# Kernel optimization log

Hardware: AMD Instinct MI355X
Metric: run time of the kernel (lower is better)

## Reference

```python
import jax, jax.numpy as jnp
import numpy as np

N_PATCHES = 14
N_BLOCKS = 12
HIDDEN = 768
N_HEADS = 12
D_HEAD = HIDDEN // N_HEADS
MLP_RATIO = 4
OUT_D = 1000
BATCH = 32
C, H, W = 3, 224, 224
PS = H // N_PATCHES            # 16
INPUT_D = C * PS * PS          # 768
SEQ = N_PATCHES ** 2 + 1       # 197
LN_EPS = 1e-5


def _pos_emb(length, d):
    i = np.arange(length, dtype=np.float64)[:, None]
    j = np.arange(d, dtype=np.float64)[None, :]
    angle = i / (10000.0 ** ((j - (j % 2)) / d))
    pe = np.where(j % 2 == 0, np.sin(angle), np.cos(angle))
    return jnp.asarray(pe, dtype=jnp.float32)  # [length, d]


def setup_inputs() -> dict:
    key = jax.random.key(0)
    ks = jax.random.split(key, 16)
    s = 0.02
    inp = {
        "x": jax.random.normal(ks[0], (BATCH, C, H, W), jnp.float32),
        "W_map": jax.random.normal(ks[1], (INPUT_D, HIDDEN), jnp.float32) * s,
        "b_map": jnp.zeros((HIDDEN,), jnp.float32),
        "cls_tok": jax.random.uniform(ks[2], (1, HIDDEN), jnp.float32),
        "pos_emb": _pos_emb(SEQ, HIDDEN),
        "ln1_s": jnp.ones((N_BLOCKS, HIDDEN), jnp.float32),
        "ln1_b": jnp.zeros((N_BLOCKS, HIDDEN), jnp.float32),
        "Wq": jax.random.normal(ks[3], (N_BLOCKS, N_HEADS, D_HEAD, D_HEAD), jnp.float32) * s,
        "bq": jnp.zeros((N_BLOCKS, N_HEADS, D_HEAD), jnp.float32),
        "Wk": jax.random.normal(ks[4], (N_BLOCKS, N_HEADS, D_HEAD, D_HEAD), jnp.float32) * s,
        "bk": jnp.zeros((N_BLOCKS, N_HEADS, D_HEAD), jnp.float32),
        "Wv": jax.random.normal(ks[5], (N_BLOCKS, N_HEADS, D_HEAD, D_HEAD), jnp.float32) * s,
        "bv": jnp.zeros((N_BLOCKS, N_HEADS, D_HEAD), jnp.float32),
        "ln2_s": jnp.ones((N_BLOCKS, HIDDEN), jnp.float32),
        "ln2_b": jnp.zeros((N_BLOCKS, HIDDEN), jnp.float32),
        "W1": jax.random.normal(ks[6], (N_BLOCKS, HIDDEN, MLP_RATIO * HIDDEN), jnp.float32) * s,
        "b1": jnp.zeros((N_BLOCKS, MLP_RATIO * HIDDEN), jnp.float32),
        "W2": jax.random.normal(ks[7], (N_BLOCKS, MLP_RATIO * HIDDEN, HIDDEN), jnp.float32) * s,
        "b2": jnp.zeros((N_BLOCKS, HIDDEN), jnp.float32),
        "W_out": jax.random.normal(ks[8], (HIDDEN, OUT_D), jnp.float32) * s,
        "b_out": jnp.zeros((OUT_D,), jnp.float32),
    }
    return inp


def _layernorm(x, scale, bias):
    m = jnp.mean(x, axis=-1, keepdims=True)
    v = jnp.mean(jnp.square(x - m), axis=-1, keepdims=True)
    return (x - m) * jax.lax.rsqrt(v + LN_EPS) * scale + bias


def _patchify(x):
    # [N,C,H,W] -> [N, np*np, C*ps*ps], channel-major flatten per patch (matches torch flatten)
    n = x.shape[0]
    p = x.reshape(n, C, N_PATCHES, PS, N_PATCHES, PS)
    p = p.transpose(0, 2, 4, 1, 3, 5)  # [N, np, np, C, ps, ps]
    return p.reshape(n, N_PATCHES * N_PATCHES, INPUT_D)


def _msa(x, Wq, bq, Wk, bk, Wv, bv):
    # x: [N,S,D]; per-head separate linears, faithful scale = 1/sqrt(n_heads)
    n, s_, _ = x.shape
    xh = x.reshape(n, s_, N_HEADS, D_HEAD)
    q = jnp.einsum('nshd,hde->nhse', xh, Wq) + bq[None, :, None, :]
    k = jnp.einsum('nshd,hde->nhse', xh, Wk) + bk[None, :, None, :]
    v = jnp.einsum('nshd,hde->nhse', xh, Wv) + bv[None, :, None, :]
    scale = 1.0 / jnp.sqrt(jnp.float32(N_HEADS))
    att = jax.nn.softmax(jnp.einsum('nhse,nhte->nhst', q, k) * scale, axis=-1)
    o = jnp.einsum('nhst,nhte->nhse', att, v)
    return o.transpose(0, 2, 1, 3).reshape(n, s_, HIDDEN)


def reference(x, W_map, b_map, cls_tok, pos_emb, ln1_s, ln1_b, Wq, bq, Wk, bk, Wv, bv,
              ln2_s, ln2_b, W1, b1, W2, b2, W_out, b_out):
    n = x.shape[0]
    tokens = _patchify(x) @ W_map + b_map                       # [N, np^2, D]
    tokens = jnp.concatenate([jnp.broadcast_to(cls_tok[None], (n, 1, HIDDEN)), tokens], axis=1)
    h = tokens + pos_emb[None]                                  # [N, S, D]
    for blk in range(N_BLOCKS):
        attn_out = _msa(_layernorm(h, ln1_s[blk], ln1_b[blk]),
                        Wq[blk], bq[blk], Wk[blk], bk[blk], Wv[blk], bv[blk])
        out = h + attn_out
        # faithful to source: MLP branch reads norm2(x), not norm2(out)
        m = _layernorm(h, ln2_s[blk], ln2_b[blk])
        m = jax.nn.gelu(m @ W1[blk] + b1[blk], approximate=False) @ W2[blk] + b2[blk]
        h = out + m
    cls = h[:, 0]                                               # [N, D]
    return jax.nn.softmax(cls @ W_out + b_out, axis=1)          # [N, out_d]
```

## Files before the change

kernel.cpp:

```cpp
#include <hip/hip_runtime.h>
#include <math.h>

#define BATCH   32
#define SEQ     197
#define HIDDEN  768
#define NHEADS  12
#define DHEAD   64
#define NBLOCKS 12
#define MLP_D   3072
#define OUTD    1000
#define NPATCH  196
#define M_TOK   (BATCH*SEQ)
#define M_PAD   6400
#define LN_EPS  1e-5f
#define SP      208

typedef _Float16 f16;
typedef _Float16 f16x8 __attribute__((ext_vector_type(8)));
typedef _Float16 f16x4 __attribute__((ext_vector_type(4)));
typedef float    f32x4 __attribute__((ext_vector_type(4)));

__device__ __forceinline__ float gelu_exact(float x) {
    return 0.5f * x * (1.0f + erff(x * 0.70710678118654752f));
}

__device__ __forceinline__ void gload_lds16(const void* g, void* l) {
    __builtin_amdgcn_global_load_lds(
        (const __attribute__((address_space(1))) void*)g,
        (__attribute__((address_space(3))) void*)l, 16, 0, 0);
}

__device__ __forceinline__ f16x8 lds_ld(const char* base, int row, int rs, int kbyte) {
    return *(const f16x8*)(base + row*rs + (kbyte ^ ((row & 7) << 4)));
}

__global__ __launch_bounds__(256) void patchify_kernel(const float* __restrict__ x,
                                                       f16* __restrict__ patches) {
    int row = blockIdx.x;
    int n = row / NPATCH;
    int p = row % NPATCH;
    int pi = p / 14, pj = p % 14;
    for (int k = threadIdx.x; k < 768; k += 256) {
        int c   = k >> 8;
        int r   = (k >> 4) & 15;
        int col = k & 15;
        patches[(size_t)row*768 + k] =
            (f16)x[(((size_t)n*3 + c)*224 + (pi*16 + r))*224 + pj*16 + col];
    }
}

__global__ __launch_bounds__(256) void convtrans_kernel(const float* __restrict__ in,
                                                        f16* __restrict__ out,
                                                        int R, int C) {
    __shared__ float tile[32][33];
    int r0 = blockIdx.y * 32, c0 = blockIdx.x * 32;
    int tx = threadIdx.x & 31, ty = threadIdx.x >> 5;
    #pragma unroll
    for (int i = 0; i < 4; ++i) {
        int r = ty + i*8;
        tile[r][tx] = in[(size_t)(r0 + r)*C + c0 + tx];
    }
    __syncthreads();
    #pragma unroll
    for (int i = 0; i < 4; ++i) {
        int r = ty + i*8;
        out[(size_t)(c0 + r)*R + r0 + tx] = (f16)tile[tx][r];
    }
}

__global__ __launch_bounds__(256) void convtrans2_kernel(const float* __restrict__ W1,
                                                         const float* __restrict__ W2,
                                                         f16* __restrict__ W1T,
                                                         f16* __restrict__ W2T) {
    int z = blockIdx.z;
    const float* in = z ? W2 : W1;
    f16* out = z ? W2T : W1T;
    int R = z ? MLP_D : HIDDEN;
    int C = z ? HIDDEN : MLP_D;
    int bx = z ? blockIdx.y : blockIdx.x;
    int by = z ? blockIdx.x : blockIdx.y;
    __shared__ float tile[32][33];
    int r0 = by * 32, c0 = bx * 32;
    int tx = threadIdx.x & 31, ty = threadIdx.x >> 5;
    #pragma unroll
    for (int i = 0; i < 4; ++i) {
        int r = ty + i*8;
        tile[r][tx] = in[(size_t)(r0 + r)*C + c0 + tx];
    }
    __syncthreads();
    #pragma unroll
    for (int i = 0; i < 4; ++i) {
        int r = ty + i*8;
        out[(size_t)(c0 + r)*R + r0 + tx] = (f16)tile[tx][r];
    }
}

__global__ __launch_bounds__(256) void qkvtrans_kernel(const float* __restrict__ Wq,
                                                       const float* __restrict__ Wk,
                                                       const float* __restrict__ Wv,
                                                       f16* __restrict__ outT) {
    int b = blockIdx.x;
    int blkL = b / 36, rem = b % 36;
    int hh = rem / 3, mat = rem % 3;
    const float* in = (mat == 0 ? Wq : mat == 1 ? Wk : Wv) + ((size_t)(blkL*12 + hh))*4096;
    f16* out = outT + (size_t)b * 4096;
    __shared__ float tile[64][65];
    int t = threadIdx.x;
    for (int i = t; i < 4096; i += 256) tile[i >> 6][i & 63] = in[i];
    __syncthreads();
    for (int i = t; i < 4096; i += 256) out[i] = (f16)tile[i & 63][i >> 6];
}

__global__ __launch_bounds__(256) void assemble_kernel(const float* __restrict__ tokens,
                                                       const float* __restrict__ cls,
                                                       const float* __restrict__ pos,
                                                       float* __restrict__ h) {
    int r = blockIdx.x;
    int n = r / SEQ, s = r % SEQ;
    for (int c = threadIdx.x; c < 768; c += 256) {
        float v = (s == 0) ? cls[c] : tokens[(size_t)(n*NPATCH + s - 1)*768 + c];
        h[(size_t)r*768 + c] = v + pos[s*768 + c];
    }
}

__global__ __launch_bounds__(256) void layernorm2_kernel(const float* __restrict__ x,
                                                         const float* __restrict__ s1,
                                                         const float* __restrict__ b1,
                                                         const float* __restrict__ s2,
                                                         const float* __restrict__ b2,
                                                         f16* __restrict__ o1,
                                                         f16* __restrict__ o2) {
    int r = blockIdx.x;
    int t = threadIdx.x;
    const float* xr = x + (size_t)r*768;
    float v0 = xr[t], v1 = xr[t+256], v2 = xr[t+512];
    float s = v0 + v1 + v2;
    #pragma unroll
    for (int off = 32; off > 0; off >>= 1) s += __shfl_xor(s, off);
    __shared__ float red[4];
    int wid = t >> 6, lane = t & 63;
    if (lane == 0) red[wid] = s;
    __syncthreads();
    float mean = (red[0]+red[1]+red[2]+red[3]) * (1.0f/768.0f);
    __syncthreads();
    float d0 = v0-mean, d1 = v1-mean, d2 = v2-mean;
    float q = d0*d0 + d1*d1 + d2*d2;
    #pragma unroll
    for (int off = 32; off > 0; off >>= 1) q += __shfl_xor(q, off);
    if (lane == 0) red[wid] = q;
    __syncthreads();
    float var = (red[0]+red[1]+red[2]+red[3]) * (1.0f/768.0f);
    float inv = rsqrtf(var + LN_EPS);
    d0 *= inv; d1 *= inv; d2 *= inv;
    f16* p1 = o1 + (size_t)r*768;
    f16* p2 = o2 + (size_t)r*768;
    p1[t]     = (f16)(d0*s1[t]     + b1[t]);
    p1[t+256] = (f16)(d1*s1[t+256] + b1[t+256]);
    p1[t+512] = (f16)(d2*s1[t+512] + b1[t+512]);
    p2[t]     = (f16)(d0*s2[t]     + b2[t]);
    p2[t+256] = (f16)(d1*s2[t+256] + b2[t+256]);
    p2[t+512] = (f16)(d2*s2[t+512] + b2[t+512]);
}

__global__ __launch_bounds__(256) void fused_attn_kernel(
        const f16* __restrict__ lnh, const f16* __restrict__ qkvT,
        const float* __restrict__ bq, const float* __restrict__ bk,
        const float* __restrict__ bv, float* __restrict__ O) {
    int n = blockIdx.x, h = blockIdx.y;
    int t = threadIdx.x, wid = t >> 6, lane = t & 63;
    int lr = lane & 15;
    int lg = lane >> 4;

    __shared__ char lds[145408];
    char* Xs  = lds;
    char* Qs  = lds + 26624;
    char* Ks  = lds + 53248;
    char* VsT = lds + 79872;
    char* Ws  = lds + 112640;
    char* Ps  = lds + 112640 + wid*8192;

    const char* xsrc = (const char*)(lnh + (size_t)n*SEQ*768 + h*64);
    for (int c = t; c < SP*8; c += 256) {
        int s = c >> 3, kb = (c & 7) * 16;
        f16x8 v = {};
        if (s < SEQ) v = *(const f16x8*)(xsrc + (size_t)s*1536 + kb);
        *(f16x8*)(Xs + s*128 + (kb ^ ((s & 7) << 4))) = v;
    }
    const char* wsrc = (const char*)(qkvT) + (size_t)h * 3 * 4096 * 2;
    for (int c = t; c < 1536; c += 256) {
        int byte = c * 16, row = byte >> 7, kb = byte & 127;
        f16x8 v = *(const f16x8*)(wsrc + byte);
        *(f16x8*)(Ws + row*128 + (kb ^ ((row & 7) << 4))) = v;
    }
    for (int c = t; c < 384; c += 256) {
        int e = c / 6, sl = c % 6;
        int kb = 416 + sl * 16;
        *(f16x8*)(VsT + e*512 + (kb ^ ((e & 7) << 4))) = (f16x8){};
    }
    __syncthreads();

    for (int idx = wid; idx < 39; idx += 4) {
        int mat = idx / 13, mt = idx % 13;
        const float* bias = (mat == 0) ? bq : (mat == 1) ? bk : bv;
        #pragma unroll
        for (int nt = 0; nt < 4; ++nt) {
            f32x4 acc = {};
            #pragma unroll
            for (int ks = 0; ks < 2; ++ks) {
                f16x8 a = lds_ld(Xs, mt*16 + lr, 128, lg*16 + ks*64);
                f16x8 b = lds_ld(Ws, mat*64 + nt*16 + lr, 128, lg*16 + ks*64);
                acc = __builtin_amdgcn_mfma_f32_16x16x32_f16(a, b, acc, 0, 0, 0);
            }
            float bb = bias[h*64 + nt*16 + lr];
            if (mat < 2) {
                char* dst = (mat == 0) ? Qs : Ks;
                #pragma unroll
                for (int j = 0; j < 4; ++j) {
                    int s = mt*16 + lg*4 + j;
                    int eb = (nt*16 + lr) * 2;
                    *(f16*)(dst + s*128 + (eb ^ ((s & 7) << 4))) = (f16)(acc[j] + bb);
                }
            } else {
                int e = nt*16 + lr;
                int sb = (mt*16 + lg*4) * 2;
                f16x4 pv;
                #pragma unroll
                for (int j = 0; j < 4; ++j) pv[j] = (f16)(acc[j] + bb);
                *(f16x4*)(VsT + e*512 + (sb ^ ((e & 7) << 4))) = pv;
            }
        }
    }
    __syncthreads();

    for (int c = lane; c < 96; c += 64) {
        int r = c / 6, kb = 416 + (c % 6) * 16;
        *(f16x8*)(Ps + r*512 + (kb ^ ((r & 7) << 4))) = (f16x8){};
    }

    const float scale = 0.28867513459481288f;
    for (int mt = wid; mt < 13; mt += 4) {
        f32x4 sacc[13];
        #pragma unroll
        for (int nt = 0; nt < 13; ++nt) sacc[nt] = (f32x4){};
        #pragma unroll
        for (int ks = 0; ks < 2; ++ks) {
            f16x8 a = lds_ld(Qs, mt*16 + lr, 128, lg*16 + ks*64);
            #pragma unroll
            for (int nt = 0; nt < 13; ++nt) {
                f16x8 b = lds_ld(Ks, nt*16 + lr, 128, lg*16 + ks*64);
                sacc[nt] = __builtin_amdgcn_mfma_f32_16x16x32_f16(a, b, sacc[nt], 0, 0, 0);
            }
        }
        float mx0 = -1e30f, mx1 = -1e30f, mx2 = -1e30f, mx3 = -1e30f;
        #pragma unroll
        for (int nt = 0; nt < 13; ++nt) {
            bool valid = (nt*16 + lr) < SEQ;
            #pragma unroll
            for (int j = 0; j < 4; ++j) {
                float v = valid ? sacc[nt][j] * scale : -1e30f;
                sacc[nt][j] = v;
            }
            mx0 = fmaxf(mx0, sacc[nt][0]); mx1 = fmaxf(mx1, sacc[nt][1]);
            mx2 = fmaxf(mx2, sacc[nt][2]); mx3 = fmaxf(mx3, sacc[nt][3]);
        }
        #pragma unroll
        for (int off = 1; off < 16; off <<= 1) {
            mx0 = fmaxf(mx0, __shfl_xor(mx0, off));
            mx1 = fmaxf(mx1, __shfl_xor(mx1, off));
            mx2 = fmaxf(mx2, __shfl_xor(mx2, off));
            mx3 = fmaxf(mx3, __shfl_xor(mx3, off));
        }
        float s0 = 0.f, s1 = 0.f, s2 = 0.f, s3 = 0.f;
        #pragma unroll
        for (int nt = 0; nt < 13; ++nt) {
            float p0 = expf(sacc[nt][0] - mx0); sacc[nt][0] = p0; s0 += p0;
            float p1 = expf(sacc[nt][1] - mx1); sacc[nt][1] = p1; s1 += p1;
            float p2 = expf(sacc[nt][2] - mx2); sacc[nt][2] = p2; s2 += p2;
            float p3 = expf(sacc[nt][3] - mx3); sacc[nt][3] = p3; s3 += p3;
        }
        #pragma unroll
        for (int off = 1; off < 16; off <<= 1) {
            s0 += __shfl_xor(s0, off); s1 += __shfl_xor(s1, off);
            s2 += __shfl_xor(s2, off); s3 += __shfl_xor(s3, off);
        }
        float i0 = 1.0f/s0, i1 = 1.0f/s1, i2 = 1.0f/s2, i3 = 1.0f/s3;
        #pragma unroll
        for (int nt = 0; nt < 13; ++nt) {
            int cb = (nt*16 + lr) * 2;
            { int r = lg*4 + 0; *(f16*)(Ps + r*512 + (cb ^ ((r & 7) << 4))) = (f16)(sacc[nt][0] * i0); }
            { int r = lg*4 + 1; *(f16*)(Ps + r*512 + (cb ^ ((r & 7) << 4))) = (f16)(sacc[nt][1] * i1); }
            { int r = lg*4 + 2; *(f16*)(Ps + r*512 + (cb ^ ((r & 7) << 4))) = (f16)(sacc[nt][2] * i2); }
            { int r = lg*4 + 3; *(f16*)(Ps + r*512 + (cb ^ ((r & 7) << 4))) = (f16)(sacc[nt][3] * i3); }
        }
        f32x4 oacc[4] = {};
        #pragma unroll
        for (int ks = 0; ks < 8; ++ks) {
            f16x8 a = lds_ld(Ps, lr, 512, lg*16 + ks*64);
            #pragma unroll
            for (int nt = 0; nt < 4; ++nt) {
                f16x8 b = lds_ld(VsT, nt*16 + lr, 512, lg*16 + ks*64);
                oacc[nt] = __builtin_amdgcn_mfma_f32_16x16x32_f16(a, b, oacc[nt], 0, 0, 0);
            }
        }
        #pragma unroll
        for (int nt = 0; nt < 4; ++nt) {
            #pragma unroll
            for (int j = 0; j < 4; ++j) {
                int s = mt*16 + lg*4 + j;
                if (s < SEQ)
                    O[((size_t)(n*SEQ + s))*768 + h*64 + nt*16 + lr] = oacc[nt][j];
            }
        }
    }
}

template<int MODE>
__global__ __launch_bounds__(256) void hgemm_kernel(
        const f16* __restrict__ A,
        const f16* __restrict__ BT,
        const float* __restrict__ bias,
        const float* __restrict__ res1,
        const float* __restrict__ res2,
        void* __restrict__ Cout, int M, int N, int K, int nbx) {
    __shared__ f16 As[2][128*64];
    __shared__ f16 Bs[2][64*64];
    int t = threadIdx.x;
    int wid = t >> 6, lane = t & 63;
    int lr = lane & 15, lg = lane >> 4;
    int wr = wid >> 1, wc = wid & 1;

    int nwg = gridDim.x, bid = blockIdx.x;
    int q = nwg >> 3, r = nwg & 7;
    int xcd = bid & 7, idx = bid >> 3;
    int swz = (xcd < r) ? xcd*(q+1) + idx : r*(q+1) + (xcd-r)*q + idx;
    int bn = (swz % nbx) * 64;
    int bm = (swz / nbx) * 128;

    int arow[4], aswk[4];
    #pragma unroll
    for (int i = 0; i < 4; ++i) {
        int fb = i*4096 + wid*1024 + lane*16;
        int row = fb >> 7, slot = (fb >> 4) & 7;
        arow[i] = row; aswk[i] = (slot ^ (row & 7)) * 8;
    }

    #define STAGE(P, K0)                                                          \
        do {                                                                      \
            _Pragma("unroll")                                                     \
            for (int i = 0; i < 4; ++i)                                           \
                gload_lds16(A + (size_t)(bm + arow[i])*K + (K0) + aswk[i],        \
                            (char*)&As[P][0] + i*4096 + wid*1024);                \
            _Pragma("unroll")                                                     \
            for (int i = 0; i < 2; ++i)                                           \
                gload_lds16(BT + (size_t)(bn + arow[i])*K + (K0) + aswk[i],       \
                            (char*)&Bs[P][0] + i*4096 + wid*1024);                \
        } while (0)

    f32x4 acc[4][2] = {};
    int nk = K >> 6;

    STAGE(0, 0);
    __syncthreads();
    for (int kt = 0; kt < nk; ++kt) {
        int cur = kt & 1;
        if (kt + 1 < nk) STAGE(cur ^ 1, (kt + 1) * 64);
        const char* Ab = (const char*)&As[cur][0];
        const char* Bb = (const char*)&Bs[cur][0];
        #pragma unroll
        for (int ks = 0; ks < 2; ++ks) {
            f16x8 a[4], b[2];
            #pragma unroll
            for (int m = 0; m < 4; ++m)
                a[m] = lds_ld(Ab, wr*64 + m*16 + lr, 128, lg*16 + ks*64);
            #pragma unroll
            for (int nn = 0; nn < 2; ++nn)
                b[nn] = lds_ld(Bb, wc*32 + nn*16 + lr, 128, lg*16 + ks*64);
            #pragma unroll
            for (int m = 0; m < 4; ++m)
                #pragma unroll
                for (int nn = 0; nn < 2; ++nn)
                    acc[m][nn] = __builtin_amdgcn_mfma_f32_16x16x32_f16(a[m], b[nn], acc[m][nn], 0, 0, 0);
        }
        __syncthreads();
    }
    #undef STAGE

    int row0 = bm + wr*64 + lg*4;
    int col0 = bn + wc*32 + lr;
    #pragma unroll
    for (int m = 0; m < 4; ++m) {
        #pragma unroll
        for (int nn = 0; nn < 2; ++nn) {
            int col = col0 + nn*16;
            float bv = bias[col];
            #pragma unroll
            for (int j = 0; j < 4; ++j) {
                int row = row0 + m*16 + j;
                if (row >= M) continue;
                float v = acc[m][nn][j] + bv;
                size_t idx = (size_t)row*N + col;
                if (MODE == 0) {
                    if (res1) v += res1[idx] + res2[idx];
                    ((float*)Cout)[idx] = v;
                } else {
                    ((f16*)Cout)[idx] = (f16)gelu_exact(v);
                }
            }
        }
    }
}

__global__ __launch_bounds__(256) void head_kernel(const float* __restrict__ h,
                                                   const float* __restrict__ W_out,
                                                   const float* __restrict__ b_out,
                                                   float* __restrict__ out) {
    int n = blockIdx.x, t = threadIdx.x;
    __shared__ float xs[HIDDEN];
    __shared__ float red[4];
    const float* hr = h + (size_t)n*SEQ*HIDDEN;
    for (int k = t; k < HIDDEN; k += 256) xs[k] = hr[k];
    __syncthreads();

    bool v3 = t < (OUTD - 768);
    int c3 = v3 ? (t + 768) : t;
    float a0 = 0.f, a1 = 0.f, a2 = 0.f, a3 = 0.f;
    #pragma unroll 8
    for (int k = 0; k < HIDDEN; ++k) {
        float xv = xs[k];
        const float* wr = W_out + (size_t)k*OUTD;
        a0 = fmaf(xv, wr[t],       a0);
        a1 = fmaf(xv, wr[t + 256], a1);
        a2 = fmaf(xv, wr[t + 512], a2);
        a3 = fmaf(xv, wr[c3],      a3);
    }
    a0 += b_out[t]; a1 += b_out[t + 256]; a2 += b_out[t + 512];
    a3 = v3 ? (a3 + b_out[t + 768]) : -1e30f;

    int wid = t >> 6, lane = t & 63;
    float mx = fmaxf(fmaxf(a0, a1), fmaxf(a2, a3));
    #pragma unroll
    for (int off = 32; off > 0; off >>= 1) mx = fmaxf(mx, __shfl_xor(mx, off));
    if (lane == 0) red[wid] = mx;
    __syncthreads();
    mx = fmaxf(fmaxf(red[0], red[1]), fmaxf(red[2], red[3]));
    __syncthreads();

    float p0 = expf(a0 - mx), p1 = expf(a1 - mx), p2 = expf(a2 - mx);
    float p3 = v3 ? expf(a3 - mx) : 0.f;
    float s = p0 + p1 + p2 + p3;
    #pragma unroll
    for (int off = 32; off > 0; off >>= 1) s += __shfl_xor(s, off);
    if (lane == 0) red[wid] = s;
    __syncthreads();
    s = red[0] + red[1] + red[2] + red[3];
    float inv = 1.0f / s;

    float* orow = out + (size_t)n*OUTD;
    orow[t]       = p0 * inv;
    orow[t + 256] = p1 * inv;
    orow[t + 512] = p2 * inv;
    if (v3) orow[t + 768] = p3 * inv;
}

extern "C" void kernel_launch(void* const* d_in, const int* in_sizes, int n_in,
                              void* d_out, int out_size, void* d_ws, size_t ws_size,
                              hipStream_t stream) {
    const float* x     = (const float*)d_in[0];
    const float* W_map = (const float*)d_in[1];
    const float* b_map = (const float*)d_in[2];
    const float* cls_t = (const float*)d_in[3];
    const float* pos   = (const float*)d_in[4];
    const float* ln1_s = (const float*)d_in[5];
    const float* ln1_b = (const float*)d_in[6];
    const float* Wq    = (const float*)d_in[7];
    const float* bq    = (const float*)d_in[8];
    const float* Wk    = (const float*)d_in[9];
    const float* bk    = (const float*)d_in[10];
    const float* Wv    = (const float*)d_in[11];
    const float* bv    = (const float*)d_in[12];
    const float* ln2_s = (const float*)d_in[13];
    const float* ln2_b = (const float*)d_in[14];
    const float* W1    = (const float*)d_in[15];
    const float* b1    = (const float*)d_in[16];
    const float* W2    = (const float*)d_in[17];
    const float* b2    = (const float*)d_in[18];
    const float* W_out = (const float*)d_in[19];
    const float* b_out = (const float*)d_in[20];
    float* out = (float*)d_out;

    char* w = (char*)d_ws;
    const size_t SZ32 = (size_t)M_TOK * HIDDEN * 4;
    float* h        = (float*)w;  w += SZ32;
    float* attn_out = (float*)w;  w += SZ32;
    f16*   mid_h    = (f16*)w;    w += (size_t)M_PAD * MLP_D * 2;
    f16*   lnh1     = (f16*)w;    w += (size_t)M_PAD * HIDDEN * 2;
    f16*   lnh2     = (f16*)w;    w += (size_t)M_PAD * HIDDEN * 2;
    f16*   W1T      = (f16*)w;    w += (size_t)MLP_D * HIDDEN * 2;
    f16*   W2T      = (f16*)w;    w += (size_t)HIDDEN * MLP_D * 2;
    f16*   WmapT    = (f16*)w;    w += (size_t)768 * 768 * 2;
    f16*   qkvT     = (f16*)w;    w += (size_t)NBLOCKS * NHEADS * 3 * 64 * 64 * 2;

    f16* patches_h = mid_h;
    patchify_kernel<<<BATCH*NPATCH, 256, 0, stream>>>(x, patches_h);
    {
        dim3 g(768/32, 768/32);
        convtrans_kernel<<<g, 256, 0, stream>>>(W_map, WmapT, 768, 768);
    }
    qkvtrans_kernel<<<NBLOCKS*NHEADS*3, 256, 0, stream>>>(Wq, Wk, Wv, qkvT);
    hgemm_kernel<0><<<49*12, 256, 0, stream>>>(patches_h, WmapT, b_map,
                                               nullptr, nullptr,
                                               (void*)attn_out, BATCH*NPATCH, 768, 768, 12);
    assemble_kernel<<<M_TOK, 256, 0, stream>>>(attn_out, cls_t, pos, h);

    for (int blk = 0; blk < NBLOCKS; ++blk) {
        layernorm2_kernel<<<M_TOK, 256, 0, stream>>>(h,
            ln1_s + blk*768, ln1_b + blk*768, ln2_s + blk*768, ln2_b + blk*768,
            lnh1, lnh2);
        {
            dim3 g(MLP_D/32, HIDDEN/32, 2);
            convtrans2_kernel<<<g, 256, 0, stream>>>(W1 + (size_t)blk*HIDDEN*MLP_D,
                                                     W2 + (size_t)blk*MLP_D*HIDDEN, W1T, W2T);
        }
        {
            dim3 g(BATCH, NHEADS);
            fused_attn_kernel<<<g, 256, 0, stream>>>(lnh1,
                qkvT + (size_t)blk*NHEADS*3*4096,
                bq + (size_t)blk*768, bk + (size_t)blk*768, bv + (size_t)blk*768,
                attn_out);
        }
        hgemm_kernel<1><<<50*48, 256, 0, stream>>>(lnh2, W1T, b1 + (size_t)blk*MLP_D,
                                                   nullptr, nullptr,
                                                   (void*)mid_h, M_TOK, MLP_D, 768, 48);
        hgemm_kernel<0><<<50*12, 256, 0, stream>>>(mid_h, W2T, b2 + (size_t)blk*HIDDEN,
                                                   h, attn_out,
                                                   (void*)h, M_TOK, HIDDEN, MLP_D, 12);
    }

    head_kernel<<<BATCH, 256, 0, stream>>>(h, W_out, b_out, out);
}
```

Baseline: 2.704 ms.

## Halve GEMM K-tile, batch all-layer weight transposes upfront, vectorize transpose kernel

The GEMM K-tile drops from 64 to 32, which halves LDS per block and is meant to raise occupancy; a new swizzled LDS layout packs two rows per 128-byte line. When the workspace is large enough, the W1/W2 transposes for all 12 layers run once before the loop instead of once per layer. The transpose kernel now uses 64x64 tiles with float4 loads and f16x4 stores. The smaller K-tile doubles the number of barriers per GEMM, and the big path depends on available workspace.

```diff
diff --git a/kernel.cpp b/kernel.cpp
--- a/kernel.cpp
+++ b/kernel.cpp
@@ -34,6 +34,12 @@
     return *(const f16x8*)(base + row*rs + (kbyte ^ ((row & 7) << 4)));
 }
 
+__device__ __forceinline__ f16x8 lds32(const char* buf, int row, int lg) {
+    int p = row >> 1;
+    int sl = (((row & 1) << 2) + lg) ^ (p & 7);
+    return *(const f16x8*)(buf + p*128 + sl*16);
+}
+
 __global__ __launch_bounds__(256) void patchify_kernel(const float* __restrict__ x,
                                                        f16* __restrict__ patches) {
     int row = blockIdx.x;
@@ -49,22 +55,28 @@
     }
 }
 
-__global__ __launch_bounds__(256) void convtrans_kernel(const float* __restrict__ in,
-                                                        f16* __restrict__ out,
-                                                        int R, int C) {
-    __shared__ float tile[32][33];
-    int r0 = blockIdx.y * 32, c0 = blockIdx.x * 32;
-    int tx = threadIdx.x & 31, ty = threadIdx.x >> 5;
+__global__ __launch_bounds__(256) void transT_kernel(const float* __restrict__ src,
+                                                     f16* __restrict__ dst,
+                                                     int R, int C) {
+    const float* in = src + (size_t)blockIdx.z * R * C;
+    f16* out = dst + (size_t)blockIdx.z * R * C;
+    __shared__ float tile[64][65];
+    int r0 = blockIdx.y * 64, c0 = blockIdx.x * 64;
+    int t = threadIdx.x;
+    int lr16 = t >> 4, lc4 = (t & 15) * 4;
     #pragma unroll
     for (int i = 0; i < 4; ++i) {
-        int r = ty + i*8;
-        tile[r][tx] = in[(size_t)(r0 + r)*C + c0 + tx];
+        int r = i*16 + lr16;
+        float4 v = *(const float4*)&in[(size_t)(r0 + r)*C + c0 + lc4];
+        tile[r][lc4] = v.x; tile[r][lc4+1] = v.y; tile[r][lc4+2] = v.z; tile[r][lc4+3] = v.w;
     }
     __syncthreads();
     #pragma unroll
     for (int i = 0; i < 4; ++i) {
-        int r = ty + i*8;
-        out[(size_t)(c0 + r)*R + r0 + tx] = (f16)tile[tx][r];
+        int c = i*16 + lr16;
+        int r = lc4;
+        f16x4 pv = { (f16)tile[r][c], (f16)tile[r+1][c], (f16)tile[r+2][c], (f16)tile[r+3][c] };
+        *(f16x4*)&out[(size_t)(c0 + c)*R + r0 + r] = pv;
     }
 }
 
@@ -322,8 +334,8 @@
         const float* __restrict__ res1,
         const float* __restrict__ res2,
         void* __restrict__ Cout, int M, int N, int K, int nbx) {
-    __shared__ f16 As[2][128*64];
-    __shared__ f16 Bs[2][64*64];
+    __shared__ f16 As[2][128*32];
+    __shared__ f16 Bs[2][64*32];
     int t = threadIdx.x;
     int wid = t >> 6, lane = t & 63;
     int lr = lane & 15, lg = lane >> 4;
@@ -336,51 +348,51 @@
     int bn = (swz % nbx) * 64;
     int bm = (swz / nbx) * 128;
 
-    int arow[4], aswk[4];
-    #pragma unroll
-    for (int i = 0; i < 4; ++i) {
+    int agrow[2], agk[2], bgrow, bgk;
+    #pragma unroll
+    for (int i = 0; i < 2; ++i) {
         int fb = i*4096 + wid*1024 + lane*16;
-        int row = fb >> 7, slot = (fb >> 4) & 7;
-        arow[i] = row; aswk[i] = (slot ^ (row & 7)) * 8;
+        int p = fb >> 7, u = ((fb >> 4) & 7) ^ (p & 7);
+        agrow[i] = 2*p + (u >> 2); agk[i] = (u & 3) * 8;
+    }
+    {
+        int fb = wid*1024 + lane*16;
+        int p = fb >> 7, u = ((fb >> 4) & 7) ^ (p & 7);
+        bgrow = 2*p + (u >> 2); bgk = (u & 3) * 8;
     }
 
     #define STAGE(P, K0)                                                          \
         do {                                                                      \
             _Pragma("unroll")                                                     \
-            for (int i = 0; i < 4; ++i)                                           \
-                gload_lds16(A + (size_t)(bm + arow[i])*K + (K0) + aswk[i],        \
+            for (int i = 0; i < 2; ++i)                                           \
+                gload_lds16(A + (size_t)(bm + agrow[i])*K + (K0) + agk[i],        \
                             (char*)&As[P][0] + i*4096 + wid*1024);                \
-            _Pragma("unroll")                                                     \
-            for (int i = 0; i < 2; ++i)                                           \
-                gload_lds16(BT + (size_t)(bn + arow[i])*K + (K0) + aswk[i],       \
-                            (char*)&Bs[P][0] + i*4096 + wid*1024);                \
+            gload_lds16(BT + (size_t)(bn + bgrow)*K + (K0) + bgk,                 \
+                        (char*)&Bs[P][0] + wid*1024);                             \
         } while (0)
 
     f32x4 acc[4][2] = {};
-    int nk = K >> 6;
+    int nk = K >> 5;
 
     STAGE(0, 0);
     __syncthreads();
     for (int kt = 0; kt < nk; ++kt) {
         int cur = kt & 1;
-        if (kt + 1 < nk) STAGE(cur ^ 1, (kt + 1) * 64);
+        if (kt + 1 < nk) STAGE(cur ^ 1, (kt + 1) * 32);
         const char* Ab = (const char*)&As[cur][0];
         const char* Bb = (const char*)&Bs[cur][0];
-        #pragma unroll
-        for (int ks = 0; ks < 2; ++ks) {
-            f16x8 a[4], b[2];
-            #pragma unroll
-            for (int m = 0; m < 4; ++m)
-                a[m] = lds_ld(Ab, wr*64 + m*16 + lr, 128, lg*16 + ks*64);
+        f16x8 a[4], b[2];
+        #pragma unroll
+        for (int m = 0; m < 4; ++m)
+            a[m] = lds32(Ab, wr*64 + m*16 + lr, lg);
+        #pragma unroll
+        for (int nn = 0; nn < 2; ++nn)
+            b[nn] = lds32(Bb, wc*32 + nn*16 + lr, lg);
+        #pragma unroll
+        for (int m = 0; m < 4; ++m)
             #pragma unroll
             for (int nn = 0; nn < 2; ++nn)
-                b[nn] = lds_ld(Bb, wc*32 + nn*16 + lr, 128, lg*16 + ks*64);
-            #pragma unroll
-            for (int m = 0; m < 4; ++m)
-                #pragma unroll
-                for (int nn = 0; nn < 2; ++nn)
-                    acc[m][nn] = __builtin_amdgcn_mfma_f32_16x16x32_f16(a[m], b[nn], acc[m][nn], 0, 0, 0);
-        }
+                acc[m][nn] = __builtin_amdgcn_mfma_f32_16x16x32_f16(a[m], b[nn], acc[m][nn], 0, 0, 0);
         __syncthreads();
     }
     #undef STAGE
@@ -488,6 +500,8 @@
     const float* b_out = (const float*)d_in[20];
     float* out = (float*)d_out;
 
+    const size_t LAYER_W = (size_t)HIDDEN * MLP_D;
+
     char* w = (char*)d_ws;
     const size_t SZ32 = (size_t)M_TOK * HIDDEN * 4;
     float* h        = (float*)w;  w += SZ32;
@@ -495,31 +509,41 @@
     f16*   mid_h    = (f16*)w;    w += (size_t)M_PAD * MLP_D * 2;
     f16*   lnh1     = (f16*)w;    w += (size_t)M_PAD * HIDDEN * 2;
     f16*   lnh2     = (f16*)w;    w += (size_t)M_PAD * HIDDEN * 2;
-    f16*   W1T      = (f16*)w;    w += (size_t)MLP_D * HIDDEN * 2;
-    f16*   W2T      = (f16*)w;    w += (size_t)HIDDEN * MLP_D * 2;
     f16*   WmapT    = (f16*)w;    w += (size_t)768 * 768 * 2;
     f16*   qkvT     = (f16*)w;    w += (size_t)NBLOCKS * NHEADS * 3 * 64 * 64 * 2;
+    size_t base_used = (size_t)(w - (char*)d_ws);
+    bool big = ws_size >= base_used + 2 * NBLOCKS * LAYER_W * 2;
+    f16* W1T = (f16*)w;  w += (big ? NBLOCKS : 1) * LAYER_W * 2;
+    f16* W2T = (f16*)w;  w += (big ? NBLOCKS : 1) * LAYER_W * 2;
 
     f16* patches_h = mid_h;
     patchify_kernel<<<BATCH*NPATCH, 256, 0, stream>>>(x, patches_h);
     {
-        dim3 g(768/32, 768/32);
-        convtrans_kernel<<<g, 256, 0, stream>>>(W_map, WmapT, 768, 768);
+        dim3 g(12, 12, 1);
+        transT_kernel<<<g, 256, 0, stream>>>(W_map, WmapT, 768, 768);
     }
     qkvtrans_kernel<<<NBLOCKS*NHEADS*3, 256, 0, stream>>>(Wq, Wk, Wv, qkvT);
+    if (big) {
+        dim3 g1(MLP_D/64, HIDDEN/64, NBLOCKS);
+        transT_kernel<<<g1, 256, 0, stream>>>(W1, W1T, HIDDEN, MLP_D);
+        dim3 g2(HIDDEN/64, MLP_D/64, NBLOCKS);
+        transT_kernel<<<g2, 256, 0, stream>>>(W2, W2T, MLP_D, HIDDEN);
+    }
     hgemm_kernel<0><<<49*12, 256, 0, stream>>>(patches_h, WmapT, b_map,
                                                nullptr, nullptr,
                                                (void*)attn_out, BATCH*NPATCH, 768, 768, 12);
     assemble_kernel<<<M_TOK, 256, 0, stream>>>(attn_out, cls_t, pos, h);
 
     for (int blk = 0; blk < NBLOCKS; ++blk) {
+        f16* w1t = big ? (W1T + (size_t)blk * LAYER_W) : W1T;
+        f16* w2t = big ? (W2T + (size_t)blk * LAYER_W) : W2T;
         layernorm2_kernel<<<M_TOK, 256, 0, stream>>>(h,
             ln1_s + blk*768, ln1_b + blk*768, ln2_s + blk*768, ln2_b + blk*768,
             lnh1, lnh2);
-        {
+        if (!big) {
             dim3 g(MLP_D/32, HIDDEN/32, 2);
-            convtrans2_kernel<<<g, 256, 0, stream>>>(W1 + (size_t)blk*HIDDEN*MLP_D,
-                                                     W2 + (size_t)blk*MLP_D*HIDDEN, W1T, W2T);
+            convtrans2_kernel<<<g, 256, 0, stream>>>(W1 + (size_t)blk*LAYER_W,
+                                                     W2 + (size_t)blk*LAYER_W, w1t, w2t);
         }
         {
             dim3 g(BATCH, NHEADS);
@@ -528,10 +552,10 @@
                 bq + (size_t)blk*768, bk + (size_t)blk*768, bv + (size_t)blk*768,
                 attn_out);
         }
-        hgemm_kernel<1><<<50*48, 256, 0, stream>>>(lnh2, W1T, b1 + (size_t)blk*MLP_D,
+        hgemm_kernel<1><<<50*48, 256, 0, stream>>>(lnh2, w1t, b1 + (size_t)blk*MLP_D,
                                                    nullptr, nullptr,
                                                    (void*)mid_h, M_TOK, MLP_D, 768, 48);
-        hgemm_kernel<0><<<50*12, 256, 0, stream>>>(mid_h, W2T, b2 + (size_t)blk*HIDDEN,
+        hgemm_kernel<0><<<50*12, 256, 0, stream>>>(mid_h, w2t, b2 + (size_t)blk*HIDDEN,
                                                    h, attn_out,
                                                    (void*)h, M_TOK, HIDDEN, MLP_D, 12);
     }
```

Result: faster. 2.612 ms (-3.4%).
